# Kernel optimization log

Measured on AMD Instinct MI355X. Metric: run time of the kernel, lower is better.

## Reference

```python
import jax, jax.numpy as jnp
import numpy as np

B, N, PD, E = 128, 512, 512, 64  # batch, n_dim, parm_dim, n_eq constraints


def setup_inputs() -> dict:
    key = jax.random.key(0)
    ks = jax.random.split(key, 6)
    x = jax.random.normal(ks[0], (B, N), jnp.float32)
    parms = jax.random.normal(ks[1], (B, PD), jnp.float32)
    W = jax.random.normal(ks[2], (N, N), jnp.float32) / np.float32(np.sqrt(N))
    M = W @ W.T  # SPD Hessian of the quadratic objective f
    A0 = jax.random.normal(ks[3], (E, N), jnp.float32) / np.float32(np.sqrt(N))
    B0 = jax.random.normal(ks[4], (E, PD), jnp.float32) / np.float32(np.sqrt(PD))
    c = jax.random.normal(ks[5], (E,), jnp.float32)
    return {"x": x, "parms": parms, "M": M, "A0": A0, "B0": B0, "c": c}


def reference(x, parms, M, A0, B0, c):
    gamma = 1.0
    b_sz, n_dim = x.shape
    n_eq = A0.shape[0]

    # unbatched objective / constraint, as passed to the torch module
    f = lambda xi, pi: 0.5 * xi @ (M @ xi) + pi @ xi
    Ffun = lambda xi, pi: A0 @ xi + B0 @ pi + c

    # vmap'd autodiff assembly, faithful to H_vec = vmap(hessian(f)) and JF = vmap(jacrev(F))
    Hfx = jax.vmap(jax.hessian(f, argnums=0))(x, parms)        # (B, N, N)
    JFx = jax.vmap(jax.jacrev(Ffun, argnums=0))(x, parms)      # (B, E, N)
    # F0 = F(0, 0) per batch element (identical rows, broadcast instead of vmap over zeros)
    F0 = Ffun(jnp.zeros((n_dim,), x.dtype), jnp.zeros((parms.shape[1],), x.dtype))
    b = -jnp.broadcast_to(F0, (b_sz, n_eq))                    # (B, E)

    Q = Hfx / 2.0
    I = jnp.eye(n_dim, dtype=x.dtype)
    At = jnp.swapaxes(JFx, 1, 2)                               # (B, N, E)
    O = jnp.zeros((b_sz, n_eq, n_eq), x.dtype)

    KKT_top = jnp.concatenate([Q + I / gamma, At], axis=2)     # (B, N, N+E)
    KKT_bot = jnp.concatenate([JFx, O], axis=2)                # (B, E, N+E)
    KKT = jnp.concatenate([KKT_top, KKT_bot], axis=1)          # (B, N+E, N+E)

    rhs_top = -parms + x / gamma                               # P = I so bmm(P/gamma, z) = z/gamma
    rhs = jnp.concatenate([rhs_top, b], axis=1)                # (B, N+E)

    sol = jnp.linalg.solve(KKT, rhs[..., None])[..., 0]        # batched dense KKT solve
    return sol[:, :n_dim]
```

## Files before the change

### kernel.cpp

```cpp
#include <hip/hip_runtime.h>
#include <math.h>

#define Bb   128
#define Nn   512
#define Ee   64
#define NCr  192
#define CGIT 22

typedef float vf4 __attribute__((ext_vector_type(4)));

struct CCoef { float cq[5], cr[5], f4, f2; };

__device__ __forceinline__ float wred(float v)
{
    #pragma unroll
    for (int s = 32; s > 0; s >>= 1) v += __shfl_xor(v, s, 64);
    return v;
}

__global__ __launch_bounds__(256) void k_prep2(const float* __restrict__ Mm,
                                               float* __restrict__ Ypart)
{
    __shared__ float As[16][68];
    __shared__ float Bs[16][68];
    const int t  = threadIdx.x;
    const int tx = t & 15, ty = t >> 4;
    const int tile = (int)(blockIdx.x >> 3);
    const int ks   = (int)(blockIdx.x & 7);
    const int r0 = (tile >> 3) * 64;
    const int c0 = (tile & 7) * 64;
    const int kbase = ks * 64;
    const int arow = t >> 2, ac4 = t & 3;

    vf4 acc0 = {0,0,0,0}, acc1 = {0,0,0,0}, acc2 = {0,0,0,0}, acc3 = {0,0,0,0};

    for (int k0 = kbase; k0 < kbase + 64; k0 += 16) {
        vf4 a = *(const vf4*)(Mm + (r0 + arow) * Nn + k0 + 4 * ac4);
        vf4 b = *(const vf4*)(Mm + (k0 + ty) * Nn + c0 + 4 * tx);
        __syncthreads();
        As[4*ac4+0][arow] = a.x; As[4*ac4+1][arow] = a.y;
        As[4*ac4+2][arow] = a.z; As[4*ac4+3][arow] = a.w;
        *(vf4*)&Bs[ty][4*tx] = b;
        __syncthreads();
        #pragma unroll
        for (int kk = 0; kk < 16; ++kk) {
            vf4 av = *(const vf4*)&As[kk][4*ty];
            vf4 bv = *(const vf4*)&Bs[kk][4*tx];
            acc0 += bv * av.x; acc1 += bv * av.y;
            acc2 += bv * av.z; acc3 += bv * av.w;
        }
    }
    float* yp = Ypart + ks * (Nn * Nn) + (r0 + 4*ty) * Nn + c0 + 4*tx;
    *(vf4*)(yp)        = acc0;
    *(vf4*)(yp + Nn)   = acc1;
    *(vf4*)(yp + 2*Nn) = acc2;
    *(vf4*)(yp + 3*Nn) = acc3;
}

__global__ __launch_bounds__(256) void k_red(const float* __restrict__ Ypart,
                                             float* __restrict__ Y)
{
    const int i4 = (int)blockIdx.x * 256 + threadIdx.x;
    vf4 s = {0,0,0,0};
    #pragma unroll
    for (int ks = 0; ks < 8; ++ks)
        s += ((const vf4*)(Ypart + ks * (Nn * Nn)))[i4];
    ((vf4*)Y)[i4] = s;
}

__global__ __launch_bounds__(1024) void k_solve(
    const float* __restrict__ x, const float* __restrict__ p,
    const float* __restrict__ Mm, const float* __restrict__ Y,
    const float* __restrict__ A0, const float* __restrict__ cvec,
    float* __restrict__ u_g, float* __restrict__ su, CCoef cf)
{
    __shared__ float L[21504];
    float* v0  = L;
    float* qb1 = L + 1024;
    float* qb2 = L + 2048;
    float* rb1 = L + 3072;
    float* rb2 = L + 4096;
    float* PQ  = L + 5120;
    float* PR  = L + 13312;

    const int t    = threadIdx.x;
    const int wg   = blockIdx.x;
    const int row0 = wg * 2;
    const int j    = t & 127;
    const int kq   = t >> 7;
    const int kb0  = kq * 64;

    {
        int m = t >> 9, n = t & 511, gr = row0 + m;
        float v = (gr < Bb) ? (x[gr * Nn + n] - p[gr * Nn + n])
                            : A0[(gr - Bb) * Nn + n];
        v0[t] = v;
        qb1[t] = cf.cq[4] * v; qb2[t] = 0.f;
        rb1[t] = cf.cr[4] * v; rb2[t] = 0.f;
    }
    __syncthreads();

    for (int step = 0; step < 4; ++step) {
        vf4 aq0 = {0,0,0,0}, aq1 = {0,0,0,0}, ar0 = {0,0,0,0}, ar1 = {0,0,0,0};
        const float* Yp = Y + kb0 * Nn + 4 * j;
        vf4 y0 = *(const vf4*)(Yp);
        vf4 y1 = *(const vf4*)(Yp + Nn);
        vf4 y2 = *(const vf4*)(Yp + 2*Nn);
        vf4 y3 = *(const vf4*)(Yp + 3*Nn);
        vf4 q0 = *(const vf4*)&qb1[kb0],  q1 = *(const vf4*)&qb1[512 + kb0];
        vf4 r0 = *(const vf4*)&rb1[kb0],  r1 = *(const vf4*)&rb1[512 + kb0];
        #pragma unroll 4
        for (int k4 = 0; k4 < 16; ++k4) {
            const int adv = (k4 < 15) ? 4 : 0;
            const float* Yn = Yp + adv * Nn;
            const int kn = kb0 + 4 * k4 + adv;
            vf4 p0 = *(const vf4*)(Yn);
            vf4 p1 = *(const vf4*)(Yn + Nn);
            vf4 p2 = *(const vf4*)(Yn + 2*Nn);
            vf4 p3 = *(const vf4*)(Yn + 3*Nn);
            vf4 nq0 = *(const vf4*)&qb1[kn], nq1 = *(const vf4*)&qb1[512 + kn];
            vf4 nr0 = *(const vf4*)&rb1[kn], nr1 = *(const vf4*)&rb1[512 + kn];
            aq0 += y0*q0.x; aq0 += y1*q0.y; aq0 += y2*q0.z; aq0 += y3*q0.w;
            aq1 += y0*q1.x; aq1 += y1*q1.y; aq1 += y2*q1.z; aq1 += y3*q1.w;
            ar0 += y0*r0.x; ar0 += y1*r0.y; ar0 += y2*r0.z; ar0 += y3*r0.w;
            ar1 += y0*r1.x; ar1 += y1*r1.y; ar1 += y2*r1.z; ar1 += y3*r1.w;
            y0 = p0; y1 = p1; y2 = p2; y3 = p3;
            q0 = nq0; q1 = nq1; r0 = nr0; r1 = nr1;
            Yp = Yn;
        }
        *(vf4*)&PQ[kq * 1024 + 4*j]       = aq0;
        *(vf4*)&PQ[kq * 1024 + 512 + 4*j] = aq1;
        *(vf4*)&PR[kq * 1024 + 4*j]       = ar0;
        *(vf4*)&PR[kq * 1024 + 512 + 4*j] = ar1;
        __syncthreads();

        {
            float yvq = 0.f, yvr = 0.f;
            #pragma unroll
            for (int pp = 0; pp < 8; ++pp) {
                yvq += PQ[pp * 1024 + t];
                yvr += PR[pp * 1024 + t];
            }
            if (step < 3) {
                float cqj = cf.cq[3 - step], crj = cf.cr[3 - step];
                float bnq = cqj * v0[t] + cf.f4 * yvq - 2.f * qb1[t] - qb2[t];
                float bnr = crj * v0[t] + cf.f4 * yvr - 2.f * rb1[t] - rb2[t];
                qb2[t] = qb1[t]; qb1[t] = bnq;
                rb2[t] = rb1[t]; rb1[t] = bnr;
            } else {
                float Fq = cf.cq[0] * v0[t] + cf.f2 * yvq - qb1[t] - qb2[t];
                float Fr = cf.cr[0] * v0[t] + cf.f2 * yvr - rb1[t] - rb2[t];
                qb1[t] = Fq; rb1[t] = Fr;
            }
        }
        __syncthreads();
    }

    {
        vf4 am0 = {0,0,0,0}, am1 = {0,0,0,0};
        const float* Mp = Mm + kb0 * Nn + 4 * j;
        vf4 y0 = *(const vf4*)(Mp);
        vf4 y1 = *(const vf4*)(Mp + Nn);
        vf4 y2 = *(const vf4*)(Mp + 2*Nn);
        vf4 y3 = *(const vf4*)(Mp + 3*Nn);
        vf4 r0 = *(const vf4*)&rb1[kb0], r1 = *(const vf4*)&rb1[512 + kb0];
        #pragma unroll 4
        for (int k4 = 0; k4 < 16; ++k4) {
            const int adv = (k4 < 15) ? 4 : 0;
            const float* Mn = Mp + adv * Nn;
            const int kn = kb0 + 4 * k4 + adv;
            vf4 p0 = *(const vf4*)(Mn);
            vf4 p1 = *(const vf4*)(Mn + Nn);
            vf4 p2 = *(const vf4*)(Mn + 2*Nn);
            vf4 p3 = *(const vf4*)(Mn + 3*Nn);
            vf4 nr0 = *(const vf4*)&rb1[kn], nr1 = *(const vf4*)&rb1[512 + kn];
            am0 += y0*r0.x; am0 += y1*r0.y; am0 += y2*r0.z; am0 += y3*r0.w;
            am1 += y0*r1.x; am1 += y1*r1.y; am1 += y2*r1.z; am1 += y3*r1.w;
            y0 = p0; y1 = p1; y2 = p2; y3 = p3;
            r0 = nr0; r1 = nr1;
            Mp = Mn;
        }
        *(vf4*)&PQ[kq * 1024 + 4*j]       = am0;
        *(vf4*)&PQ[kq * 1024 + 512 + 4*j] = am1;
        __syncthreads();
        {
            float s = qb1[t];
            #pragma unroll
            for (int pp = 0; pp < 8; ++pp) s += PQ[pp * 1024 + t];
            v0[t] = s;
            u_g[(row0 + (t >> 9)) * Nn + (t & 511)] = s;
        }
        __syncthreads();
    }

    {
        float* As = L + 1024;
        float* Ps = L + 3328;
        float accS = 0.f;
        const int e = t & 63;
        const int sub = t >> 6;
        const int m_ = sub & 1, ch = sub >> 1;
        for (int k0 = 0; k0 < Nn; k0 += 32) {
            __syncthreads();
            for (int i = t; i < 2048; i += 1024) {
                int ee = i >> 5, cc = i & 31;
                As[ee * 33 + cc] = A0[ee * Nn + k0 + cc];
            }
            __syncthreads();
            #pragma unroll
            for (int cc = 0; cc < 4; ++cc)
                accS += As[e * 33 + ch * 4 + cc] * v0[m_ * 512 + k0 + ch * 4 + cc];
        }
        Ps[sub * 64 + e] = accS;
        __syncthreads();
        if (t < 128) {
            int mm = t >> 6, ee = t & 63;
            float val = 0.f;
            #pragma unroll
            for (int c2 = 0; c2 < 8; ++c2) val += Ps[(mm + 2 * c2) * 64 + ee];
            int gr = row0 + mm;
            int jj = (gr < Bb) ? (64 + gr) : (gr - Bb);
            su[ee * NCr + jj] = val + ((jj >= 64) ? cvec[ee] : 0.f);
        }
    }
}

__global__ __launch_bounds__(512) void k_lam_final(
    const float* __restrict__ u_g, const float* __restrict__ su,
    float* __restrict__ out)
{
    __shared__ float Sm[64][65];
    __shared__ float pb[8][64];
    const int t = threadIdx.x, w = t >> 6, lane = t & 63;

    for (int i = t; i < 64 * 64; i += 512)
        Sm[i >> 6][i & 63] = su[(i >> 6) * NCr + (i & 63)];
    __syncthreads();

    const int b = blockIdx.x * 8 + w;
    float srow[64];
    #pragma unroll
    for (int k = 0; k < 64; ++k) srow[k] = Sm[lane][k];

    float rhs = su[lane * NCr + 64 + b];
    float xv = 0.f, rv = rhs, pv = rv;
    float rr = wred(rv * rv);
    for (int itc = 0; itc < CGIT; ++itc) {
        pb[w][lane] = pv;
        float q = 0.f;
        #pragma unroll
        for (int k = 0; k < 64; ++k) q += srow[k] * pb[w][k];
        float pq = wred(pv * q);
        float alpha = rr / fmaxf(pq, 1e-30f);
        xv += alpha * pv;
        rv -= alpha * q;
        float rr2 = wred(rv * rv);
        float beta = rr2 / fmaxf(rr, 1e-30f);
        rr = rr2;
        pv = rv + beta * pv;
    }
    pb[w][lane] = xv;

    #pragma unroll
    for (int i = 0; i < 8; ++i) {
        int n = lane + 64 * i;
        float acc = u_g[b * Nn + n];
        #pragma unroll 4
        for (int e = 0; e < Ee; ++e)
            acc -= pb[w][e] * u_g[(Bb + e) * Nn + n];
        out[b * Nn + n] = acc;
    }
}

extern "C" void kernel_launch(void* const* d_in, const int* in_sizes, int n_in,
                              void* d_out, int out_size, void* d_ws, size_t ws_size,
                              hipStream_t stream)
{
    const float* x     = (const float*)d_in[0];
    const float* parms = (const float*)d_in[1];
    const float* Mm    = (const float*)d_in[2];
    const float* A0    = (const float*)d_in[3];
    const float* c     = (const float*)d_in[5];
    float* out = (float*)d_out;

    float* ws    = (float*)d_ws;
    float* Y     = ws;
    float* Ypart = ws + Nn * Nn;
    float* u_g   = ws + Nn * Nn + 8 * Nn * Nn;
    float* su    = u_g + NCr * Nn;

    const double aa = 1.0, bbound = 3.12;
    const double th = 0.5 * (bbound + aa), de = 0.5 * (bbound - aa), sg = th / de;
    double rp[16] = {0}, dp[16] = {0}, xp[16] = {0}, hd[16];
    rp[0] = 1.0; dp[0] = 1.0 / th; xp[0] = 1.0 / th;
    double rho_prev = 1.0 / sg;
    for (int k = 1; k <= 9; ++k) {
        double rho = 1.0 / (2.0 * sg - rho_prev);
        double C1 = rho * rho_prev, C2 = 2.0 * rho / de;
        for (int i = 15; i >= 1; --i) hd[i] = dp[i - 1];
        hd[0] = 0.0;
        for (int i = 0; i < 16; ++i) {
            rp[i] -= hd[i];
            dp[i] = C1 * dp[i] + C2 * rp[i];
            xp[i] += dp[i];
        }
        rho_prev = rho;
    }
    double pm[16] = {0};
    for (int k = 0; k <= 9; ++k) {
        double term[16] = {0}; term[0] = 1.0;
        for (int e = 0; e < k; ++e) {
            double nt[16] = {0};
            for (int i = 0; i <= e; ++i) { nt[i] += term[i]; nt[i + 1] += 0.5 * term[i]; }
            for (int i = 0; i <= e + 1; ++i) term[i] = nt[i];
        }
        for (int i = 0; i <= k; ++i) pm[i] += xp[k] * term[i];
    }
    double qm[8] = {0}, rm[8] = {0};
    for (int jj = 0; jj < 5; ++jj) { qm[jj] = pm[2 * jj]; rm[jj] = pm[2 * jj + 1]; }
    const double mmax = 2.0 * (bbound - 1.0);
    const double ymax = mmax * mmax;
    double cq[5] = {0}, cr[5] = {0};
    const int NP = 64;
    for (int i = 0; i < NP; ++i) {
        double thn = M_PI * (i + 0.5) / NP;
        double s = cos(thn);
        double y = 0.5 * ymax * (s + 1.0);
        double vq = 0, vr = 0;
        for (int d2 = 4; d2 >= 0; --d2) { vq = vq * y + qm[d2]; vr = vr * y + rm[d2]; }
        for (int jj = 0; jj < 5; ++jj) {
            cq[jj] += (2.0 / NP) * vq * cos(jj * thn);
            cr[jj] += (2.0 / NP) * vr * cos(jj * thn);
        }
    }
    cq[0] *= 0.5; cr[0] *= 0.5;
    CCoef cf;
    for (int jj = 0; jj < 5; ++jj) { cf.cq[jj] = (float)cq[jj]; cf.cr[jj] = (float)cr[jj]; }
    cf.f4 = (float)(4.0 / ymax);
    cf.f2 = (float)(2.0 / ymax);

    hipLaunchKernelGGL(k_prep2,     dim3(512), dim3(256),  0, stream, Mm, Ypart);
    hipLaunchKernelGGL(k_red,       dim3(256), dim3(256),  0, stream, Ypart, Y);
    hipLaunchKernelGGL(k_solve,     dim3(96),  dim3(1024), 0, stream,
                       x, parms, Mm, Y, A0, c, u_g, su, cf);
    hipLaunchKernelGGL(k_lam_final, dim3(16),  dim3(512),  0, stream, u_g, su, out);
}
```

Measured before the change: 190.6 us.

## Split monolithic solve into tiled batched GEMM kernels per Chebyshev step

The single 96-block solve kernel, which streamed Y from global memory once per row pair, is replaced by a sequence of launches. The Chebyshev recurrence now runs as shared-memory tiled GEMMs over all 384 stacked rows with split-K partials, followed by elementwise update kernels. The final M multiply and the A0·u product move to separate tiled kernels. Reuse of Y across rows should improve and parallelism should rise, at the cost of about ten extra launches and round trips of partial sums through global memory.

```diff
diff --git a/kernel.cpp b/kernel.cpp
--- a/kernel.cpp
+++ b/kernel.cpp
@@ -5,6 +5,7 @@
 #define Nn   512
 #define Ee   64
 #define NCr  192
+#define NR2  384
 #define CGIT 22
 
 typedef float vf4 __attribute__((ext_vector_type(4)));
@@ -68,161 +69,131 @@
     ((vf4*)Y)[i4] = s;
 }
 
-__global__ __launch_bounds__(1024) void k_solve(
+__global__ __launch_bounds__(256) void k_build(
     const float* __restrict__ x, const float* __restrict__ p,
-    const float* __restrict__ Mm, const float* __restrict__ Y,
-    const float* __restrict__ A0, const float* __restrict__ cvec,
-    float* __restrict__ u_g, float* __restrict__ su, CCoef cf)
-{
-    __shared__ float L[21504];
-    float* v0  = L;
-    float* qb1 = L + 1024;
-    float* qb2 = L + 2048;
-    float* rb1 = L + 3072;
-    float* rb2 = L + 4096;
-    float* PQ  = L + 5120;
-    float* PR  = L + 13312;
-
-    const int t    = threadIdx.x;
-    const int wg   = blockIdx.x;
-    const int row0 = wg * 2;
-    const int j    = t & 127;
-    const int kq   = t >> 7;
-    const int kb0  = kq * 64;
-
-    {
-        int m = t >> 9, n = t & 511, gr = row0 + m;
-        float v = (gr < Bb) ? (x[gr * Nn + n] - p[gr * Nn + n])
-                            : A0[(gr - Bb) * Nn + n];
-        v0[t] = v;
-        qb1[t] = cf.cq[4] * v; qb2[t] = 0.f;
-        rb1[t] = cf.cr[4] * v; rb2[t] = 0.f;
-    }
-    __syncthreads();
-
-    for (int step = 0; step < 4; ++step) {
-        vf4 aq0 = {0,0,0,0}, aq1 = {0,0,0,0}, ar0 = {0,0,0,0}, ar1 = {0,0,0,0};
-        const float* Yp = Y + kb0 * Nn + 4 * j;
-        vf4 y0 = *(const vf4*)(Yp);
-        vf4 y1 = *(const vf4*)(Yp + Nn);
-        vf4 y2 = *(const vf4*)(Yp + 2*Nn);
-        vf4 y3 = *(const vf4*)(Yp + 3*Nn);
-        vf4 q0 = *(const vf4*)&qb1[kb0],  q1 = *(const vf4*)&qb1[512 + kb0];
-        vf4 r0 = *(const vf4*)&rb1[kb0],  r1 = *(const vf4*)&rb1[512 + kb0];
-        #pragma unroll 4
-        for (int k4 = 0; k4 < 16; ++k4) {
-            const int adv = (k4 < 15) ? 4 : 0;
-            const float* Yn = Yp + adv * Nn;
-            const int kn = kb0 + 4 * k4 + adv;
-            vf4 p0 = *(const vf4*)(Yn);
-            vf4 p1 = *(const vf4*)(Yn + Nn);
-            vf4 p2 = *(const vf4*)(Yn + 2*Nn);
-            vf4 p3 = *(const vf4*)(Yn + 3*Nn);
-            vf4 nq0 = *(const vf4*)&qb1[kn], nq1 = *(const vf4*)&qb1[512 + kn];
-            vf4 nr0 = *(const vf4*)&rb1[kn], nr1 = *(const vf4*)&rb1[512 + kn];
-            aq0 += y0*q0.x; aq0 += y1*q0.y; aq0 += y2*q0.z; aq0 += y3*q0.w;
-            aq1 += y0*q1.x; aq1 += y1*q1.y; aq1 += y2*q1.z; aq1 += y3*q1.w;
-            ar0 += y0*r0.x; ar0 += y1*r0.y; ar0 += y2*r0.z; ar0 += y3*r0.w;
-            ar1 += y0*r1.x; ar1 += y1*r1.y; ar1 += y2*r1.z; ar1 += y3*r1.w;
-            y0 = p0; y1 = p1; y2 = p2; y3 = p3;
-            q0 = nq0; q1 = nq1; r0 = nr0; r1 = nr1;
-            Yp = Yn;
-        }
-        *(vf4*)&PQ[kq * 1024 + 4*j]       = aq0;
-        *(vf4*)&PQ[kq * 1024 + 512 + 4*j] = aq1;
-        *(vf4*)&PR[kq * 1024 + 4*j]       = ar0;
-        *(vf4*)&PR[kq * 1024 + 512 + 4*j] = ar1;
-        __syncthreads();
-
-        {
-            float yvq = 0.f, yvr = 0.f;
-            #pragma unroll
-            for (int pp = 0; pp < 8; ++pp) {
-                yvq += PQ[pp * 1024 + t];
-                yvr += PR[pp * 1024 + t];
-            }
-            if (step < 3) {
-                float cqj = cf.cq[3 - step], crj = cf.cr[3 - step];
-                float bnq = cqj * v0[t] + cf.f4 * yvq - 2.f * qb1[t] - qb2[t];
-                float bnr = crj * v0[t] + cf.f4 * yvr - 2.f * rb1[t] - rb2[t];
-                qb2[t] = qb1[t]; qb1[t] = bnq;
-                rb2[t] = rb1[t]; rb1[t] = bnr;
-            } else {
-                float Fq = cf.cq[0] * v0[t] + cf.f2 * yvq - qb1[t] - qb2[t];
-                float Fr = cf.cr[0] * v0[t] + cf.f2 * yvr - rb1[t] - rb2[t];
-                qb1[t] = Fq; rb1[t] = Fr;
-            }
-        }
-        __syncthreads();
-    }
-
-    {
-        vf4 am0 = {0,0,0,0}, am1 = {0,0,0,0};
-        const float* Mp = Mm + kb0 * Nn + 4 * j;
-        vf4 y0 = *(const vf4*)(Mp);
-        vf4 y1 = *(const vf4*)(Mp + Nn);
-        vf4 y2 = *(const vf4*)(Mp + 2*Nn);
-        vf4 y3 = *(const vf4*)(Mp + 3*Nn);
-        vf4 r0 = *(const vf4*)&rb1[kb0], r1 = *(const vf4*)&rb1[512 + kb0];
-        #pragma unroll 4
-        for (int k4 = 0; k4 < 16; ++k4) {
-            const int adv = (k4 < 15) ? 4 : 0;
-            const float* Mn = Mp + adv * Nn;
-            const int kn = kb0 + 4 * k4 + adv;
-            vf4 p0 = *(const vf4*)(Mn);
-            vf4 p1 = *(const vf4*)(Mn + Nn);
-            vf4 p2 = *(const vf4*)(Mn + 2*Nn);
-            vf4 p3 = *(const vf4*)(Mn + 3*Nn);
-            vf4 nr0 = *(const vf4*)&rb1[kn], nr1 = *(const vf4*)&rb1[512 + kn];
-            am0 += y0*r0.x; am0 += y1*r0.y; am0 += y2*r0.z; am0 += y3*r0.w;
-            am1 += y0*r1.x; am1 += y1*r1.y; am1 += y2*r1.z; am1 += y3*r1.w;
-            y0 = p0; y1 = p1; y2 = p2; y3 = p3;
-            r0 = nr0; r1 = nr1;
-            Mp = Mn;
-        }
-        *(vf4*)&PQ[kq * 1024 + 4*j]       = am0;
-        *(vf4*)&PQ[kq * 1024 + 512 + 4*j] = am1;
-        __syncthreads();
-        {
-            float s = qb1[t];
-            #pragma unroll
-            for (int pp = 0; pp < 8; ++pp) s += PQ[pp * 1024 + t];
-            v0[t] = s;
-            u_g[(row0 + (t >> 9)) * Nn + (t & 511)] = s;
-        }
-        __syncthreads();
-    }
-
-    {
-        float* As = L + 1024;
-        float* Ps = L + 3328;
-        float accS = 0.f;
-        const int e = t & 63;
-        const int sub = t >> 6;
-        const int m_ = sub & 1, ch = sub >> 1;
-        for (int k0 = 0; k0 < Nn; k0 += 32) {
-            __syncthreads();
-            for (int i = t; i < 2048; i += 1024) {
-                int ee = i >> 5, cc = i & 31;
-                As[ee * 33 + cc] = A0[ee * Nn + k0 + cc];
-            }
-            __syncthreads();
-            #pragma unroll
-            for (int cc = 0; cc < 4; ++cc)
-                accS += As[e * 33 + ch * 4 + cc] * v0[m_ * 512 + k0 + ch * 4 + cc];
-        }
-        Ps[sub * 64 + e] = accS;
-        __syncthreads();
-        if (t < 128) {
-            int mm = t >> 6, ee = t & 63;
-            float val = 0.f;
-            #pragma unroll
-            for (int c2 = 0; c2 < 8; ++c2) val += Ps[(mm + 2 * c2) * 64 + ee];
-            int gr = row0 + mm;
-            int jj = (gr < Bb) ? (64 + gr) : (gr - Bb);
-            su[ee * NCr + jj] = val + ((jj >= 64) ? cvec[ee] : 0.f);
-        }
-    }
+    const float* __restrict__ A0,
+    float* __restrict__ v0, float* __restrict__ B1s, float* __restrict__ B2s,
+    float cq4, float cr4)
+{
+    const int i = (int)blockIdx.x * 256 + threadIdx.x;
+    const int row = i >> 9;
+    float v = (row < Bb) ? (x[i] - p[i]) : A0[i - Bb * Nn];
+    v0[i] = v;
+    B1s[i]            = cq4 * v;
+    B1s[i + NCr * Nn] = cr4 * v;
+    B2s[i]            = 0.f;
+    B2s[i + NCr * Nn] = 0.f;
+}
+
+__global__ __launch_bounds__(256) void k_ymul(const float* __restrict__ src,
+                                              const float* __restrict__ mat,
+                                              float* __restrict__ part)
+{
+    __shared__ float As[16][68];
+    __shared__ float Bs[16][68];
+    const int t  = threadIdx.x;
+    const int tx = t & 15, ty = t >> 4;
+    const int wg = (int)blockIdx.x;
+    const int ks  = wg & 7;
+    const int cb  = (wg >> 3) & 7;
+    const int rbk = wg >> 6;
+    const int r0 = rbk * 64, c0 = cb * 64, kbase = ks * 64;
+    const int arow = t >> 2, ac4 = t & 3;
+
+    vf4 acc0 = {0,0,0,0}, acc1 = {0,0,0,0}, acc2 = {0,0,0,0}, acc3 = {0,0,0,0};
+
+    for (int k0 = kbase; k0 < kbase + 64; k0 += 16) {
+        vf4 a = *(const vf4*)(src + (r0 + arow) * Nn + k0 + 4 * ac4);
+        vf4 b = *(const vf4*)(mat + (k0 + ty) * Nn + c0 + 4 * tx);
+        __syncthreads();
+        As[4*ac4+0][arow] = a.x; As[4*ac4+1][arow] = a.y;
+        As[4*ac4+2][arow] = a.z; As[4*ac4+3][arow] = a.w;
+        *(vf4*)&Bs[ty][4*tx] = b;
+        __syncthreads();
+        #pragma unroll
+        for (int kk = 0; kk < 16; ++kk) {
+            vf4 av = *(const vf4*)&As[kk][4*ty];
+            vf4 bv = *(const vf4*)&Bs[kk][4*tx];
+            acc0 += bv * av.x; acc1 += bv * av.y;
+            acc2 += bv * av.z; acc3 += bv * av.w;
+        }
+    }
+    float* yp = part + ks * (NR2 * Nn) + (r0 + 4*ty) * Nn + c0 + 4*tx;
+    *(vf4*)(yp)        = acc0;
+    *(vf4*)(yp + Nn)   = acc1;
+    *(vf4*)(yp + 2*Nn) = acc2;
+    *(vf4*)(yp + 3*Nn) = acc3;
+}
+
+__global__ __launch_bounds__(256) void k_upd(
+    const float* __restrict__ part, const float* __restrict__ v0,
+    float* __restrict__ B1s, float* __restrict__ B2s,
+    float cqj, float crj, float fscale, int finalstep)
+{
+    const int i = (int)blockIdx.x * 256 + threadIdx.x;
+    float yvq = 0.f, yvr = 0.f;
+    #pragma unroll
+    for (int ks = 0; ks < 8; ++ks) {
+        yvq += part[ks * (NR2 * Nn) + i];
+        yvr += part[ks * (NR2 * Nn) + NCr * Nn + i];
+    }
+    float v  = v0[i];
+    float q1 = B1s[i], q2 = B2s[i];
+    float r1 = B1s[i + NCr * Nn], r2 = B2s[i + NCr * Nn];
+    if (!finalstep) {
+        float bnq = cqj * v + fscale * yvq - 2.f * q1 - q2;
+        float bnr = crj * v + fscale * yvr - 2.f * r1 - r2;
+        B2s[i] = q1;              B1s[i] = bnq;
+        B2s[i + NCr * Nn] = r1;   B1s[i + NCr * Nn] = bnr;
+    } else {
+        float Fq = cqj * v + fscale * yvq - q1 - q2;
+        float Fr = crj * v + fscale * yvr - r1 - r2;
+        B1s[i] = Fq;              B1s[i + NCr * Nn] = Fr;
+    }
+}
+
+__global__ __launch_bounds__(256) void k_ufin(
+    const float* __restrict__ part, const float* __restrict__ B1s,
+    float* __restrict__ u_g)
+{
+    const int i = (int)blockIdx.x * 256 + threadIdx.x;
+    float s = B1s[i];
+    #pragma unroll
+    for (int ks = 0; ks < 8; ++ks)
+        s += part[ks * (NR2 * Nn) + i];
+    u_g[i] = s;
+}
+
+__global__ __launch_bounds__(256) void k_small(
+    const float* __restrict__ A0, const float* __restrict__ u,
+    const float* __restrict__ c, float* __restrict__ su)
+{
+    __shared__ float As[16][33];
+    __shared__ float Us[16][33];
+    int t  = threadIdx.x;
+    int tx = t & 15, ty = t >> 4;
+    int e0 = ((int)blockIdx.x / 12) * 16;
+    int j0 = ((int)blockIdx.x % 12) * 16;
+    float acc = 0.f;
+
+    for (int k0 = 0; k0 < Nn; k0 += 32) {
+        #pragma unroll
+        for (int i = 0; i < 2; ++i) {
+            int ii = t + i * 256;
+            int rr = ii >> 5, cc = ii & 31;
+            As[rr][cc] = A0[(e0 + rr) * Nn + k0 + cc];
+            int j_ = j0 + rr;
+            int urow = (j_ < 64) ? (Bb + j_) : (j_ - 64);
+            Us[rr][cc] = u[urow * Nn + k0 + cc];
+        }
+        __syncthreads();
+        #pragma unroll
+        for (int kk = 0; kk < 32; ++kk)
+            acc += As[ty][kk] * Us[tx][kk];
+        __syncthreads();
+    }
+    int e = e0 + ty, j = j0 + tx;
+    su[e * NCr + j] = acc + ((j >= 64) ? c[e] : 0.f);
 }
 
 __global__ __launch_bounds__(512) void k_lam_final(
@@ -237,7 +208,7 @@
         Sm[i >> 6][i & 63] = su[(i >> 6) * NCr + (i & 63)];
     __syncthreads();
 
-    const int b = blockIdx.x * 8 + w;
+    const int b = (int)blockIdx.x * 8 + w;
     float srow[64];
     #pragma unroll
     for (int k = 0; k < 64; ++k) srow[k] = Sm[lane][k];
@@ -284,9 +255,13 @@
     float* out = (float*)d_out;
 
     float* ws    = (float*)d_ws;
-    float* Y     = ws;
-    float* Ypart = ws + Nn * Nn;
-    float* u_g   = ws + Nn * Nn + 8 * Nn * Nn;
+    float* Ypart = ws;
+    float* Y     = Ypart + 8 * Nn * Nn;
+    float* Zpart = Y + Nn * Nn;
+    float* v0    = Zpart + 8 * NR2 * Nn;
+    float* B1s   = v0 + NCr * Nn;
+    float* B2s   = B1s + NR2 * Nn;
+    float* u_g   = B2s + NR2 * Nn;
     float* su    = u_g + NCr * Nn;
 
     const double aa = 1.0, bbound = 3.12;
@@ -339,9 +314,29 @@
     cf.f4 = (float)(4.0 / ymax);
     cf.f2 = (float)(2.0 / ymax);
 
-    hipLaunchKernelGGL(k_prep2,     dim3(512), dim3(256),  0, stream, Mm, Ypart);
-    hipLaunchKernelGGL(k_red,       dim3(256), dim3(256),  0, stream, Ypart, Y);
-    hipLaunchKernelGGL(k_solve,     dim3(96),  dim3(1024), 0, stream,
-                       x, parms, Mm, Y, A0, c, u_g, su, cf);
-    hipLaunchKernelGGL(k_lam_final, dim3(16),  dim3(512),  0, stream, u_g, su, out);
-}
+    hipLaunchKernelGGL(k_prep2, dim3(512), dim3(256), 0, stream, Mm, Ypart);
+    hipLaunchKernelGGL(k_red,   dim3(256), dim3(256), 0, stream, Ypart, Y);
+    hipLaunchKernelGGL(k_build, dim3(384), dim3(256), 0, stream,
+                       x, parms, A0, v0, B1s, B2s, cf.cq[4], cf.cr[4]);
+
+    for (int step = 0; step < 4; ++step) {
+        hipLaunchKernelGGL(k_ymul, dim3(NR2 / 64 * 64), dim3(256), 0, stream,
+                           B1s, Y, Zpart);
+        if (step < 3) {
+            hipLaunchKernelGGL(k_upd, dim3(384), dim3(256), 0, stream,
+                               Zpart, v0, B1s, B2s,
+                               cf.cq[3 - step], cf.cr[3 - step], cf.f4, 0);
+        } else {
+            hipLaunchKernelGGL(k_upd, dim3(384), dim3(256), 0, stream,
+                               Zpart, v0, B1s, B2s,
+                               cf.cq[0], cf.cr[0], cf.f2, 1);
+        }
+    }
+
+    hipLaunchKernelGGL(k_ymul, dim3(192), dim3(256), 0, stream,
+                       B1s + NCr * Nn, Mm, Zpart);
+    hipLaunchKernelGGL(k_ufin, dim3(384), dim3(256), 0, stream, Zpart, B1s, u_g);
+
+    hipLaunchKernelGGL(k_small,     dim3(48), dim3(256), 0, stream, A0, u_g, c, su);
+    hipLaunchKernelGGL(k_lam_final, dim3(16), dim3(512), 0, stream, u_g, su, out);
+}
```

Result: slower. 194.5 us (+2.0%).
